# Performance work log

Hardware: AMD Instinct MI355X
Metric: run time of the kernel (lower is better)

## Reference

```python
import jax, jax.numpy as jnp
import numpy as np

NEG_INF = -1e10  # matches the -10000000000.0 additive mask in the torch source


def setup_inputs() -> dict:
    key = jax.random.key(0)
    k1, k2, k3, k4 = jax.random.split(key, 4)
    bs, h, S, d = 4, 16, 2048, 64
    bs_h = bs * h
    query = jax.random.normal(k1, (bs_h, S, d), dtype=jnp.float32)
    key_t = jax.random.normal(k2, (bs_h, S, d), dtype=jnp.float32)
    value = jax.random.normal(k3, (bs_h, S, d), dtype=jnp.float32)
    attn_mask = jax.random.randint(k4, (bs, S), 0, 2).astype(jnp.int32)
    return {"query": query, "key": key_t, "value": value,
            "attn_mask": attn_mask, "decod_mask": 1}


def reference(query, key, value, attn_mask, decod_mask):
    bs_h, K, d_k = key.shape
    Q = query.shape[1]
    bs = attn_mask.shape[0]
    h = bs_h // bs

    # scores: [bs_h, Q, K]
    scores = jnp.einsum('bqd,bkd->bqk', query, key) / jnp.sqrt(
        jnp.asarray(d_k, dtype=query.dtype))

    # padding mask: positions where attn_mask == 0 get -1e10.
    # torch repeats the [bs, Q, K] mask h times along the batch axis
    # (order: [mask; mask; ...]), i.e. batch index b in bs_h maps to b % bs.
    pad = (attn_mask == 0).astype(scores.dtype) * NEG_INF  # [bs, K]
    scores = (scores.reshape(h, bs, Q, K) + pad[None, :, None, :]).reshape(bs_h, Q, K)

    if decod_mask is not None:
        causal = jnp.triu(jnp.full((Q, K), NEG_INF, dtype=scores.dtype), k=1)
        scores = scores + causal[None, :, :]

    attn = jax.nn.softmax(scores, axis=-1)
    # dropout p=0.0 -> identity
    return jnp.einsum('bqk,bkd->bqd', attn, value)
```

## Files before the change

kernel.cpp:

```cpp
#include <hip/hip_runtime.h>
#include <hip/hip_bf16.h>

#define S_LEN 2048
#define DH 64
#define NBATCH 4
#define LOG2E 1.44269504088896f
#define SCL2E 0.18033688011112042f
#define PADC  (-1.44269504088896e10f)
#define NEG_BIG -1e10f
#define NEG_CAUSAL -3.0e38f

typedef __attribute__((ext_vector_type(8))) short short8;
typedef __attribute__((ext_vector_type(4))) float floatx4;
typedef __attribute__((ext_vector_type(4))) unsigned uintx4;

__device__ inline float fast_exp2(float x) {
#if __has_builtin(__builtin_amdgcn_exp2f)
  return __builtin_amdgcn_exp2f(x);
#else
  return exp2f(x);
#endif
}

__device__ inline short f2bf(float x) {
  union { float f; unsigned u; } v; v.f = x;
  unsigned r = v.u + 0x7fffu + ((v.u >> 16) & 1u);
  return (short)(r >> 16);
}

__device__ inline short8 pack8(float4 a, float4 b) {
  short8 r;
  r[0] = f2bf(a.x); r[1] = f2bf(a.y); r[2] = f2bf(a.z); r[3] = f2bf(a.w);
  r[4] = f2bf(b.x); r[5] = f2bf(b.y); r[6] = f2bf(b.z); r[7] = f2bf(b.w);
  return r;
}

__device__ inline unsigned packhi(unsigned hi, unsigned lo) {
#if __has_builtin(__builtin_amdgcn_perm)
  return __builtin_amdgcn_perm(hi, lo, 0x07060302u);
#else
  return (hi & 0xFFFF0000u) | (lo >> 16);
#endif
}

#define MFMA32(a, b, c) __builtin_amdgcn_mfma_f32_16x16x32_bf16(a, b, c, 0, 0, 0)

__global__ void zero_sums(float* __restrict__ s) {
  s[blockIdx.x * 256 + threadIdx.x] = 0.f;
}

__global__ void prep_kv(const float* __restrict__ Kg, const float* __restrict__ Vg,
                        short8* __restrict__ Kf, short8* __restrict__ Vf,
                        const int* __restrict__ maskg, float* __restrict__ sums) {
  const int gid = (int)blockIdx.x;
  if (gid < 4096) {
    const int idx = gid * 256 + (int)threadIdx.x;
    const int lane = idx & 63;
    const int t = idx >> 6;
    const int nt = t & 3, ks = (t >> 2) & 1;
    const int kt = (t >> 3) & 31;
    const int bh = t >> 8;
    const int c = lane & 15, g = lane >> 4;
    const float* src = Kg + ((size_t)bh * S_LEN + kt * 64 + nt * 16 + c) * DH + ks * 32 + g * 8;
    float4 a = *(const float4*)src;
    float4 b = *(const float4*)(src + 4);
    Kf[idx] = pack8(a, b);
  } else {
    const int idx = (gid - 4096) * 256 + (int)threadIdx.x;
    const int lane = idx & 63;
    const int t = idx >> 6;
    const int dt = t & 3, nt2 = (t >> 2) & 1;
    const int kt = (t >> 3) & 31;
    const int bh = t >> 8;
    const int b = bh & (NBATCH - 1);
    const int c = lane & 15, g = lane >> 4;
    const int key0 = kt * 64 + nt2 * 32 + g * 4;
    const float* src = Vg + ((size_t)bh * S_LEN + key0) * DH + dt * 16 + c;
    int4 m0 = *(const int4*)&maskg[b * S_LEN + key0];
    int4 m1 = *(const int4*)&maskg[b * S_LEN + key0 + 16];
    short8 r;
    float s = 0.f;
    {
      float v0 = src[(size_t)0 * DH], v1 = src[(size_t)1 * DH];
      float v2 = src[(size_t)2 * DH], v3 = src[(size_t)3 * DH];
      r[0] = f2bf(v0); r[1] = f2bf(v1); r[2] = f2bf(v2); r[3] = f2bf(v3);
      s += (m0.x ? v0 : 0.f) + (m0.y ? v1 : 0.f) + (m0.z ? v2 : 0.f) + (m0.w ? v3 : 0.f);
    }
    {
      float v0 = src[(size_t)16 * DH], v1 = src[(size_t)17 * DH];
      float v2 = src[(size_t)18 * DH], v3 = src[(size_t)19 * DH];
      r[4] = f2bf(v0); r[5] = f2bf(v1); r[6] = f2bf(v2); r[7] = f2bf(v3);
      s += (m1.x ? v0 : 0.f) + (m1.y ? v1 : 0.f) + (m1.z ? v2 : 0.f) + (m1.w ? v3 : 0.f);
    }
    Vf[idx] = r;
    s += __shfl_xor(s, 16);
    s += __shfl_xor(s, 32);
    if (lane < 16) atomicAdd(&sums[bh * 64 + dt * 16 + lane], s);
  }
}

__device__ __forceinline__ void loadk(const short8* __restrict__ kbase, int kt,
                                      int lane, short8 (&dst)[8]) {
  const short8* p = kbase + ((size_t)kt * 8) * 64 + lane;
#pragma unroll
  for (int i = 0; i < 8; ++i) dst[i] = p[i * 64];
}

__device__ __forceinline__ void compute_tile(
    int kt, int qbase, int b, int c, int g, int lane,
    const short8 (&kf)[8], const short8 (&qf)[2][2], const short8& ones,
    const int* __restrict__ maskg, const short8* __restrict__ vbase,
    floatx4 (&acc)[2][4], floatx4 (&acc_l)[2])
{
  int4 mv[4];
#pragma unroll
  for (int nt = 0; nt < 4; ++nt)
    mv[nt] = *(const int4*)&maskg[b * S_LEN + kt * 64 + nt * 16 + g * 4];

  short8 vf[8];
  {
    const short8* vp = vbase + ((size_t)kt * 8) * 64 + lane;
#pragma unroll
    for (int i = 0; i < 8; ++i) vf[i] = vp[i * 64];
  }

  floatx4 padv[4];
#pragma unroll
  for (int nt = 0; nt < 4; ++nt) {
    padv[nt][0] = mv[nt].x ? 0.f : PADC;
    padv[nt][1] = mv[nt].y ? 0.f : PADC;
    padv[nt][2] = mv[nt].z ? 0.f : PADC;
    padv[nt][3] = mv[nt].w ? 0.f : PADC;
  }

#pragma unroll
  for (int s2 = 0; s2 < 2; ++s2) {
    if (kt * 64 > qbase + s2 * 16 + 15) continue;
    floatx4 st[4];
    __builtin_amdgcn_s_setprio(1);
#pragma unroll
    for (int nt = 0; nt < 4; ++nt) {
      floatx4 cc = (floatx4){0.f, 0.f, 0.f, 0.f};
      cc = MFMA32(kf[nt],     qf[s2][0], cc);
      cc = MFMA32(kf[4 + nt], qf[s2][1], cc);
      st[nt] = cc;
    }
    __builtin_amdgcn_s_setprio(0);
    const int q = qbase + s2 * 16 + c;
    const bool causal = (kt * 64 + 63) > (qbase + s2 * 16);
    unsigned pu[4][4];
#pragma unroll
    for (int nt = 0; nt < 4; ++nt) {
#pragma unroll
      for (int r = 0; r < 4; ++r) {
        float arg = fmaf(st[nt][r], SCL2E, padv[nt][r]);
        if (causal) {
          const int key = kt * 64 + nt * 16 + g * 4 + r;
          arg = (key > q) ? NEG_CAUSAL : arg;
        }
        pu[nt][r] = __float_as_uint(fast_exp2(arg)) + 0x8000u;
      }
    }
    short8 pP[2];
#pragma unroll
    for (int nt2 = 0; nt2 < 2; ++nt2) {
      uintx4 wv;
      wv[0] = packhi(pu[2 * nt2][1],     pu[2 * nt2][0]);
      wv[1] = packhi(pu[2 * nt2][3],     pu[2 * nt2][2]);
      wv[2] = packhi(pu[2 * nt2 + 1][1], pu[2 * nt2 + 1][0]);
      wv[3] = packhi(pu[2 * nt2 + 1][3], pu[2 * nt2 + 1][2]);
      pP[nt2] = __builtin_bit_cast(short8, wv);
    }
    __builtin_amdgcn_s_setprio(1);
#pragma unroll
    for (int nt2 = 0; nt2 < 2; ++nt2) {
      acc_l[s2] = MFMA32(pP[nt2], ones, acc_l[s2]);
#pragma unroll
      for (int dt = 0; dt < 4; ++dt)
        acc[s2][dt] = MFMA32(pP[nt2], vf[nt2 * 4 + dt], acc[s2][dt]);
    }
    __builtin_amdgcn_s_setprio(0);
  }
}

__global__ __launch_bounds__(256, 2) void flash_fwd3(
    const float* __restrict__ Qg, const int* __restrict__ maskg,
    const short8* __restrict__ KfB, const short8* __restrict__ VfB,
    float* __restrict__ Og)
{
  const int bh = blockIdx.x;
  const int b  = bh & (NBATCH - 1);
  const int tid = (int)threadIdx.x;
  const int w = tid >> 6, lane = tid & 63;
  const int widx = (int)blockIdx.y * 4 + w;
  const int c = lane & 15, g = lane >> 4;

  const short8 ones = {0x3F80, 0x3F80, 0x3F80, 0x3F80, 0x3F80, 0x3F80, 0x3F80, 0x3F80};
  const short8* kbase = KfB + (size_t)bh * 32 * 8 * 64;
  const short8* vbase = VfB + (size_t)bh * 32 * 8 * 64;

#pragma unroll
  for (int half = 0; half < 2; ++half) {
    const int ch = half ? (63 - widx) : widx;
    const int qbase = ch * 32;
    const int ktmax = ch >> 1;

    short8 qf[2][2];
#pragma unroll
    for (int s2 = 0; s2 < 2; ++s2) {
      const float* qp = Qg + ((size_t)bh * S_LEN + qbase + s2 * 16 + c) * DH + g * 8;
#pragma unroll
      for (int ks = 0; ks < 2; ++ks) {
        float4 a  = *(const float4*)(qp + ks * 32);
        float4 b4 = *(const float4*)(qp + ks * 32 + 4);
        qf[s2][ks] = pack8(a, b4);
      }
    }

    floatx4 acc[2][4];
    floatx4 acc_l[2];
#pragma unroll
    for (int s2 = 0; s2 < 2; ++s2) {
      acc_l[s2] = (floatx4){0.f, 0.f, 0.f, 0.f};
#pragma unroll
      for (int dt = 0; dt < 4; ++dt) acc[s2][dt] = (floatx4){0.f, 0.f, 0.f, 0.f};
    }

    short8 kfA[8], kfB_[8];
    loadk(kbase, 0, lane, kfA);
    for (int kt = 0; kt <= ktmax; kt += 2) {
      const bool hasB = (kt + 1 <= ktmax);
      if (hasB) loadk(kbase, kt + 1, lane, kfB_);
      compute_tile(kt, qbase, b, c, g, lane, kfA, qf, ones, maskg, vbase, acc, acc_l);
      if (hasB) {
        if (kt + 2 <= ktmax) loadk(kbase, kt + 2, lane, kfA);
        compute_tile(kt + 1, qbase, b, c, g, lane, kfB_, qf, ones, maskg, vbase, acc, acc_l);
      }
    }

#pragma unroll
    for (int s2 = 0; s2 < 2; ++s2) {
      float rr[4];
#pragma unroll
      for (int r = 0; r < 4; ++r) rr[r] = 1.f / acc_l[s2][r];
#pragma unroll
      for (int dt = 0; dt < 4; ++dt)
#pragma unroll
        for (int r = 0; r < 4; ++r)
          Og[((size_t)bh * S_LEN + qbase + s2 * 16 + g * 4 + r) * DH + dt * 16 + c] =
              acc[s2][dt][r] * rr[r];
    }
  }
}

__global__ void fixup_write(const float* __restrict__ Vg, const int* __restrict__ maskg,
                            const float* __restrict__ sums, float* __restrict__ Og)
{
  const int bh = blockIdx.x;
  const int b  = bh & (NBATCH - 1);
  const int d  = (int)threadIdx.x;
  int fmin = S_LEN, n = 0;
  for (int k = d; k < S_LEN; k += 64) {
    if (maskg[b * S_LEN + k] != 0) { ++n; if (k < fmin) fmin = k; }
  }
#pragma unroll
  for (int off = 1; off < 64; off <<= 1) {
    fmin = min(fmin, __shfl_xor(fmin, off));
    n += __shfl_xor(n, off);
  }
  if (fmin == 0) return;
  const float ms = sums[bh * 64 + d];
  float pre = 0.f;
  for (int q = 0; q < fmin; ++q) {
    pre += Vg[((size_t)bh * S_LEN + q) * DH + d];
    Og[((size_t)bh * S_LEN + q) * DH + d] = (pre + ms) / (float)(q + 1 + n);
  }
}

__global__ __launch_bounds__(256, 2) void flash_fwd_lds(
    const float* __restrict__ Qg, const float* __restrict__ Kg,
    const float* __restrict__ Vg, const int* __restrict__ maskg,
    float* __restrict__ Og)
{
  const int qt  = blockIdx.x;
  const int bh  = blockIdx.y;
  const int b   = bh & (NBATCH - 1);
  const int tid = (int)threadIdx.x;
  const int w = tid >> 6, lane = tid & 63;
  const int g = lane >> 4, c = lane & 15;

  __shared__ __align__(16) short Ks[64 * 72];
  __shared__ __align__(16) short Vt[64 * 72];
  __shared__ __align__(16) short Ps[4][32 * 72];

  short8 qf[2][2];
#pragma unroll
  for (int s2 = 0; s2 < 2; ++s2) {
    const float* qp = Qg + ((size_t)bh * S_LEN + qt * 128 + w * 32 + s2 * 16 + c) * DH + g * 8;
#pragma unroll
    for (int ks = 0; ks < 2; ++ks) {
      float4 a  = *(const float4*)(qp + ks * 32);
      float4 bq = *(const float4*)(qp + ks * 32 + 4);
      qf[s2][ks] = pack8(a, bq);
    }
  }

  floatx4 acc[2][4];
  float mrow[2][4], lrow[2][4];
#pragma unroll
  for (int s2 = 0; s2 < 2; ++s2) {
#pragma unroll
    for (int i = 0; i < 4; ++i) acc[s2][i] = (floatx4){0.f, 0.f, 0.f, 0.f};
#pragma unroll
    for (int r = 0; r < 4; ++r) { mrow[s2][r] = -3.4e38f; lrow[s2][r] = 0.f; }
  }

  const int rstage = tid >> 2;
  const int dstage = (tid & 3) * 16;
  const int ktmax = 2 * qt + 1;

  for (int kt = 0; kt <= ktmax; ++kt) {
    __syncthreads();
    {
      const size_t rowbase = ((size_t)bh * S_LEN + kt * 64 + rstage) * DH + dstage;
      const float* kp = Kg + rowbase;
      const float* vp = Vg + rowbase;
      float4 k0 = *(const float4*)kp;       float4 k1 = *(const float4*)(kp + 4);
      float4 k2 = *(const float4*)(kp + 8); float4 k3 = *(const float4*)(kp + 12);
      *(short8*)&Ks[rstage * 72 + dstage]     = pack8(k0, k1);
      *(short8*)&Ks[rstage * 72 + dstage + 8] = pack8(k2, k3);
      float4 v0 = *(const float4*)vp;       float4 v1 = *(const float4*)(vp + 4);
      float4 v2 = *(const float4*)(vp + 8); float4 v3 = *(const float4*)(vp + 12);
      float vv[16] = {v0.x, v0.y, v0.z, v0.w, v1.x, v1.y, v1.z, v1.w,
                      v2.x, v2.y, v2.z, v2.w, v3.x, v3.y, v3.z, v3.w};
#pragma unroll
      for (int i = 0; i < 16; ++i) Vt[(dstage + i) * 72 + rstage] = f2bf(vv[i]);
    }
    __syncthreads();

    float padv[4];
#pragma unroll
    for (int nt = 0; nt < 4; ++nt)
      padv[nt] = (maskg[b * S_LEN + kt * 64 + nt * 16 + c] != 0) ? 0.f : NEG_BIG;

    short8 kf[2][4];
#pragma unroll
    for (int ks = 0; ks < 2; ++ks)
#pragma unroll
      for (int nt = 0; nt < 4; ++nt)
        kf[ks][nt] = *(const short8*)&Ks[(nt * 16 + c) * 72 + ks * 32 + g * 8];

    bool act[2];
#pragma unroll
    for (int s2 = 0; s2 < 2; ++s2)
      act[s2] = (kt * 64) <= (qt * 128 + w * 32 + s2 * 16 + 15);

#pragma unroll
    for (int s2 = 0; s2 < 2; ++s2) {
      if (!act[s2]) continue;
      floatx4 sv[4];
#pragma unroll
      for (int nt = 0; nt < 4; ++nt) {
        floatx4 cc = (floatx4){0.f, 0.f, 0.f, 0.f};
        cc = MFMA32(qf[s2][0], kf[0][nt], cc);
        cc = MFMA32(qf[s2][1], kf[1][nt], cc);
        sv[nt] = cc;
      }
      const int qrow0 = qt * 128 + w * 32 + s2 * 16 + g * 4;
#pragma unroll
      for (int nt = 0; nt < 4; ++nt) {
        const int key = kt * 64 + nt * 16 + c;
#pragma unroll
        for (int r = 0; r < 4; ++r) {
          float s = sv[nt][r] * 0.125f + padv[nt];
          if (key > qrow0 + r) s = NEG_CAUSAL;
          sv[nt][r] = s;
        }
      }
#pragma unroll
      for (int r = 0; r < 4; ++r) {
        float mx = fmaxf(fmaxf(sv[0][r], sv[1][r]), fmaxf(sv[2][r], sv[3][r]));
        mx = fmaxf(mx, __shfl_xor(mx, 1));
        mx = fmaxf(mx, __shfl_xor(mx, 2));
        mx = fmaxf(mx, __shfl_xor(mx, 4));
        mx = fmaxf(mx, __shfl_xor(mx, 8));
        const float mold = mrow[s2][r];
        const float mnew = fmaxf(mold, mx);
        const float corr = fast_exp2((mold - mnew) * LOG2E);
        float ps = 0.f;
#pragma unroll
        for (int nt = 0; nt < 4; ++nt) {
          float p = fast_exp2((sv[nt][r] - mnew) * LOG2E);
          sv[nt][r] = p;
          ps += p;
        }
        ps += __shfl_xor(ps, 1);
        ps += __shfl_xor(ps, 2);
        ps += __shfl_xor(ps, 4);
        ps += __shfl_xor(ps, 8);
        lrow[s2][r] = lrow[s2][r] * corr + ps;
        mrow[s2][r] = mnew;
#pragma unroll
        for (int dt = 0; dt < 4; ++dt) acc[s2][dt][r] *= corr;
      }
#pragma unroll
      for (int nt = 0; nt < 4; ++nt)
#pragma unroll
        for (int r = 0; r < 4; ++r)
          Ps[w][(s2 * 16 + g * 4 + r) * 72 + nt * 16 + c] = f2bf(sv[nt][r]);
    }

#pragma unroll
    for (int ks = 0; ks < 2; ++ks) {
      short8 pf0 = {}, pf1 = {};
      if (act[0]) pf0 = *(const short8*)&Ps[w][c * 72 + ks * 32 + g * 8];
      if (act[1]) pf1 = *(const short8*)&Ps[w][(16 + c) * 72 + ks * 32 + g * 8];
#pragma unroll
      for (int dt = 0; dt < 4; ++dt) {
        short8 vfr = *(const short8*)&Vt[(dt * 16 + c) * 72 + ks * 32 + g * 8];
        if (act[0]) acc[0][dt] = MFMA32(pf0, vfr, acc[0][dt]);
        if (act[1]) acc[1][dt] = MFMA32(pf1, vfr, acc[1][dt]);
      }
    }
  }

#pragma unroll
  for (int s2 = 0; s2 < 2; ++s2) {
    float rl[4];
#pragma unroll
    for (int r = 0; r < 4; ++r) rl[r] = 1.f / lrow[s2][r];
    const size_t obase = ((size_t)bh * S_LEN + qt * 128 + w * 32 + s2 * 16 + g * 4) * DH + c;
#pragma unroll
    for (int dt = 0; dt < 4; ++dt)
#pragma unroll
      for (int r = 0; r < 4; ++r)
        Og[obase + (size_t)r * DH + dt * 16] = acc[s2][dt][r] * rl[r];
  }
}

__global__ void fixup(const float* __restrict__ Vg, const int* __restrict__ maskg,
                      float* __restrict__ Og)
{
  const int bh = blockIdx.x;
  const int b  = bh & (NBATCH - 1);
  const int tid = (int)threadIdx.x;
  __shared__ int sFirst;
  __shared__ float4 sRed[64][16];
  __shared__ int sCnt[64];
  if (tid == 0) sFirst = S_LEN;
  __syncthreads();
  for (int k = tid; k < S_LEN; k += 1024)
    if (maskg[b * S_LEN + k] != 0) atomicMin(&sFirst, k);
  __syncthreads();
  const int f = sFirst;
  if (f == 0) return;

  const int dq = tid & 15, kg = tid >> 4;
  float4 a = {0.f, 0.f, 0.f, 0.f}; int cnt = 0;
  for (int k = kg; k < S_LEN; k += 64) {
    if (maskg[b * S_LEN + k] != 0) {
      float4 v = *(const float4*)&Vg[((size_t)bh * S_LEN + k) * DH + dq * 4];
      a.x += v.x; a.y += v.y; a.z += v.z; a.w += v.w; cnt++;
    }
  }
  sRed[kg][dq] = a;
  if (dq == 0) sCnt[kg] = cnt;
  __syncthreads();
  if (tid < 64) {
    const int q4 = tid >> 2, e = tid & 3;
    float ms = 0.f; int n = 0;
#pragma unroll 4
    for (int i = 0; i < 64; ++i) {
      const float* p4 = (const float*)&sRed[i][q4];
      ms += p4[e];
      n += sCnt[i];
    }
    float pre = 0.f;
    for (int q = 0; q < f; ++q) {
      pre += Vg[((size_t)bh * S_LEN + q) * DH + tid];
      Og[((size_t)bh * S_LEN + q) * DH + tid] = (pre + ms) / (float)(q + 1 + n);
    }
  }
}

extern "C" void kernel_launch(void* const* d_in, const int* in_sizes, int n_in,
                              void* d_out, int out_size, void* d_ws, size_t ws_size,
                              hipStream_t stream) {
  const float* Q = (const float*)d_in[0];
  const float* K = (const float*)d_in[1];
  const float* V = (const float*)d_in[2];
  const int* mask = (const int*)d_in[3];
  float* O = (float*)d_out;

  const size_t KF_BYTES = (size_t)64 * S_LEN * DH * 2;
  const size_t SUM_BYTES = (size_t)64 * 64 * sizeof(float);
  if (ws_size >= 2 * KF_BYTES + SUM_BYTES) {
    short8* Kf = (short8*)d_ws;
    short8* Vf = (short8*)((char*)d_ws + KF_BYTES);
    float* sums = (float*)((char*)d_ws + 2 * KF_BYTES);
    zero_sums<<<dim3(16), dim3(256), 0, stream>>>(sums);
    prep_kv<<<dim3(8192), dim3(256), 0, stream>>>(K, V, Kf, Vf, mask, sums);
    flash_fwd3<<<dim3(64, 8), dim3(256), 0, stream>>>(Q, mask, Kf, Vf, O);
    fixup_write<<<dim3(64), dim3(64), 0, stream>>>(V, mask, sums, O);
  } else {
    flash_fwd_lds<<<dim3(16, 64), dim3(256), 0, stream>>>(Q, K, V, mask, O);
    fixup<<<dim3(64), dim3(1024), 0, stream>>>(V, mask, O);
  }
}
```

Before: 203.2 us.

## Split key tiles across two wave groups and merge partial results in LDS

After: 678.5 us. +233.9%, slower.

```diff
diff --git a/kernel.cpp b/kernel.cpp
--- a/kernel.cpp
+++ b/kernel.cpp
@@ -183,7 +183,7 @@
   }
 }
 
-__global__ __launch_bounds__(256, 2) void flash_fwd3(
+__global__ __launch_bounds__(512, 4) void flash_fwd4(
     const float* __restrict__ Qg, const int* __restrict__ maskg,
     const short8* __restrict__ KfB, const short8* __restrict__ VfB,
     float* __restrict__ Og)
@@ -192,8 +192,13 @@
   const int b  = bh & (NBATCH - 1);
   const int tid = (int)threadIdx.x;
   const int w = tid >> 6, lane = tid & 63;
-  const int widx = (int)blockIdx.y * 4 + w;
+  const int p4 = w & 3;
+  const int h  = w >> 2;
+  const int widx = (int)blockIdx.y * 4 + p4;
   const int c = lane & 15, g = lane >> 4;
+
+  __shared__ float sAcc[4][32 * 65];
+  __shared__ float sL[4][32];
 
   const short8 ones = {0x3F80, 0x3F80, 0x3F80, 0x3F80, 0x3F80, 0x3F80, 0x3F80, 0x3F80};
   const short8* kbase = KfB + (size_t)bh * 32 * 8 * 64;
@@ -227,29 +232,49 @@
     }
 
     short8 kfA[8], kfB_[8];
-    loadk(kbase, 0, lane, kfA);
-    for (int kt = 0; kt <= ktmax; kt += 2) {
-      const bool hasB = (kt + 1 <= ktmax);
-      if (hasB) loadk(kbase, kt + 1, lane, kfB_);
+    loadk(kbase, h, lane, kfA);
+    for (int kt = h; kt <= ktmax; kt += 4) {
+      const bool hasB = (kt + 2 <= ktmax);
+      if (hasB) loadk(kbase, kt + 2, lane, kfB_);
       compute_tile(kt, qbase, b, c, g, lane, kfA, qf, ones, maskg, vbase, acc, acc_l);
       if (hasB) {
-        if (kt + 2 <= ktmax) loadk(kbase, kt + 2, lane, kfA);
-        compute_tile(kt + 1, qbase, b, c, g, lane, kfB_, qf, ones, maskg, vbase, acc, acc_l);
-      }
-    }
-
-#pragma unroll
-    for (int s2 = 0; s2 < 2; ++s2) {
-      float rr[4];
-#pragma unroll
-      for (int r = 0; r < 4; ++r) rr[r] = 1.f / acc_l[s2][r];
-#pragma unroll
-      for (int dt = 0; dt < 4; ++dt)
+        if (kt + 4 <= ktmax) loadk(kbase, kt + 4, lane, kfA);
+        compute_tile(kt + 2, qbase, b, c, g, lane, kfB_, qf, ones, maskg, vbase, acc, acc_l);
+      }
+    }
+
+    if (h == 0) {
+#pragma unroll
+      for (int s2 = 0; s2 < 2; ++s2) {
+#pragma unroll
+        for (int dt = 0; dt < 4; ++dt)
+#pragma unroll
+          for (int r = 0; r < 4; ++r)
+            sAcc[p4][(s2 * 16 + g * 4 + r) * 65 + dt * 16 + c] = acc[s2][dt][r];
+        if (c == 0)
+#pragma unroll
+          for (int r = 0; r < 4; ++r) sL[p4][s2 * 16 + g * 4 + r] = acc_l[s2][r];
+      }
+    }
+    __syncthreads();
+    if (h == 1) {
+#pragma unroll
+      for (int s2 = 0; s2 < 2; ++s2) {
+        float rr[4];
 #pragma unroll
         for (int r = 0; r < 4; ++r)
-          Og[((size_t)bh * S_LEN + qbase + s2 * 16 + g * 4 + r) * DH + dt * 16 + c] =
-              acc[s2][dt][r] * rr[r];
-    }
+          rr[r] = 1.f / (acc_l[s2][r] + sL[p4][s2 * 16 + g * 4 + r]);
+#pragma unroll
+        for (int dt = 0; dt < 4; ++dt)
+#pragma unroll
+          for (int r = 0; r < 4; ++r) {
+            float o = acc[s2][dt][r] + sAcc[p4][(s2 * 16 + g * 4 + r) * 65 + dt * 16 + c];
+            Og[((size_t)bh * S_LEN + qbase + s2 * 16 + g * 4 + r) * DH + dt * 16 + c] =
+                o * rr[r];
+          }
+      }
+    }
+    __syncthreads();
   }
 }
 
@@ -500,7 +525,7 @@
     float* sums = (float*)((char*)d_ws + 2 * KF_BYTES);
     zero_sums<<<dim3(16), dim3(256), 0, stream>>>(sums);
     prep_kv<<<dim3(8192), dim3(256), 0, stream>>>(K, V, Kf, Vf, mask, sums);
-    flash_fwd3<<<dim3(64, 8), dim3(256), 0, stream>>>(Q, mask, Kf, Vf, O);
+    flash_fwd4<<<dim3(64, 8), dim3(512), 0, stream>>>(Q, mask, Kf, Vf, O);
     fixup_write<<<dim3(64), dim3(64), 0, stream>>>(V, mask, sums, O);
   } else {
     flash_fwd_lds<<<dim3(16, 64), dim3(256), 0, stream>>>(Q, K, V, mask, O);
```

## Replace static causal pairing with atomic ticket work queue, longest chunks first

Applied to the files above, without the earlier changes.

After: 638.4 us. 3.14x slower.

```diff
diff --git a/kernel.cpp b/kernel.cpp
--- a/kernel.cpp
+++ b/kernel.cpp
@@ -45,8 +45,9 @@
 
 #define MFMA32(a, b, c) __builtin_amdgcn_mfma_f32_16x16x32_bf16(a, b, c, 0, 0, 0)
 
-__global__ void zero_sums(float* __restrict__ s) {
-  s[blockIdx.x * 256 + threadIdx.x] = 0.f;
+__global__ void zero_sums(unsigned* __restrict__ s) {
+  const unsigned i = blockIdx.x * 256 + threadIdx.x;
+  if (i < 4096 + 64) s[i] = 0u;
 }
 
 __global__ void prep_kv(const float* __restrict__ Kg, const float* __restrict__ Vg,
@@ -183,27 +184,30 @@
   }
 }
 
-__global__ __launch_bounds__(256, 2) void flash_fwd3(
+__global__ __launch_bounds__(256, 4) void flash_fwd5(
     const float* __restrict__ Qg, const int* __restrict__ maskg,
     const short8* __restrict__ KfB, const short8* __restrict__ VfB,
-    float* __restrict__ Og)
+    float* __restrict__ Og, int* __restrict__ ticket)
 {
-  const int bh = blockIdx.x;
-  const int b  = bh & (NBATCH - 1);
   const int tid = (int)threadIdx.x;
-  const int w = tid >> 6, lane = tid & 63;
-  const int widx = (int)blockIdx.y * 4 + w;
+  const int lane = tid & 63;
   const int c = lane & 15, g = lane >> 4;
 
   const short8 ones = {0x3F80, 0x3F80, 0x3F80, 0x3F80, 0x3F80, 0x3F80, 0x3F80, 0x3F80};
-  const short8* kbase = KfB + (size_t)bh * 32 * 8 * 64;
-  const short8* vbase = VfB + (size_t)bh * 32 * 8 * 64;
-
-#pragma unroll
-  for (int half = 0; half < 2; ++half) {
-    const int ch = half ? (63 - widx) : widx;
+
+  for (;;) {
+    int t = 0;
+    if (lane == 0) t = atomicAdd(ticket, 1);
+    t = __builtin_amdgcn_readfirstlane(t);
+    if (t >= 64 * 64) break;
+
+    const int bh = t & 63;
+    const int ch = 63 - (t >> 6);
+    const int b  = bh & (NBATCH - 1);
     const int qbase = ch * 32;
     const int ktmax = ch >> 1;
+    const short8* kbase = KfB + (size_t)bh * 32 * 8 * 64;
+    const short8* vbase = VfB + (size_t)bh * 32 * 8 * 64;
 
     short8 qf[2][2];
 #pragma unroll
@@ -493,14 +497,15 @@
   float* O = (float*)d_out;
 
   const size_t KF_BYTES = (size_t)64 * S_LEN * DH * 2;
-  const size_t SUM_BYTES = (size_t)64 * 64 * sizeof(float);
+  const size_t SUM_BYTES = (size_t)(4096 + 64) * sizeof(float);
   if (ws_size >= 2 * KF_BYTES + SUM_BYTES) {
     short8* Kf = (short8*)d_ws;
     short8* Vf = (short8*)((char*)d_ws + KF_BYTES);
     float* sums = (float*)((char*)d_ws + 2 * KF_BYTES);
-    zero_sums<<<dim3(16), dim3(256), 0, stream>>>(sums);
+    int* ticket = (int*)((char*)d_ws + 2 * KF_BYTES + 4096 * sizeof(float));
+    zero_sums<<<dim3(17), dim3(256), 0, stream>>>((unsigned*)sums);
     prep_kv<<<dim3(8192), dim3(256), 0, stream>>>(K, V, Kf, Vf, mask, sums);
-    flash_fwd3<<<dim3(64, 8), dim3(256), 0, stream>>>(Q, mask, Kf, Vf, O);
+    flash_fwd5<<<dim3(1024), dim3(256), 0, stream>>>(Q, mask, Kf, Vf, O, ticket);
     fixup_write<<<dim3(64), dim3(64), 0, stream>>>(V, mask, sums, O);
   } else {
     flash_fwd_lds<<<dim3(16, 64), dim3(256), 0, stream>>>(Q, K, V, mask, O);
```
